# Kernel tuning notes

Measured on AMD Instinct MI355X. Metric: run time of the kernel, lower is better.

## Reference

```python
import jax, jax.numpy as jnp
import numpy as np

V, NJ, NSHAPE, NEXP, B = 5023, 5, 100, 50, 1024
PARENTS = np.array([-1, 0, 1, 1, 1])  # FLAME kinematic tree: global, neck, jaw, eyeL, eyeR


def rodrigues(rot_vecs):
    """Axis-angle [..., 3] -> rotation matrices [..., 3, 3] (SMPL-style, eps-safe)."""
    angle = jnp.linalg.norm(rot_vecs + 1e-8, axis=-1, keepdims=True)  # [...,1]
    axis = rot_vecs / angle
    cos = jnp.cos(angle)[..., None]
    sin = jnp.sin(angle)[..., None]
    rx, ry, rz = axis[..., 0], axis[..., 1], axis[..., 2]
    z = jnp.zeros_like(rx)
    K = jnp.stack([z, -rz, ry, rz, z, -rx, -ry, rx, z], axis=-1).reshape(rot_vecs.shape[:-1] + (3, 3))
    eye = jnp.eye(3, dtype=rot_vecs.dtype)
    return eye + sin * K + (1.0 - cos) * (K @ K)


def setup_inputs() -> dict:
    ks = jax.random.split(jax.random.key(0), 8)
    shape_params = jax.random.normal(ks[0], (B, NSHAPE), jnp.float32)
    expression_params = jax.random.normal(ks[1], (B, NEXP), jnp.float32)
    pose_params = 0.1 * jax.random.normal(ks[2], (B, 6), jnp.float32)
    v_template = jax.random.normal(ks[3], (V, 3), jnp.float32)
    shapedirs = 0.01 * jax.random.normal(ks[4], (V, 3, NSHAPE + NEXP), jnp.float32)
    posedirs = 0.01 * jax.random.normal(ks[5], ((NJ - 1) * 9, V * 3), jnp.float32)
    jr = jax.random.uniform(ks[6], (NJ, V), jnp.float32)
    J_regressor = jr / jr.sum(axis=1, keepdims=True)
    w = jax.random.uniform(ks[7], (V, NJ), jnp.float32)
    lbs_weights = w / w.sum(axis=1, keepdims=True)
    return dict(shape_params=shape_params, expression_params=expression_params,
                pose_params=pose_params, v_template=v_template, shapedirs=shapedirs,
                posedirs=posedirs, J_regressor=J_regressor, lbs_weights=lbs_weights)


def reference(shape_params, expression_params, pose_params, v_template,
              shapedirs, posedirs, J_regressor, lbs_weights):
    b = shape_params.shape[0]
    dt = shape_params.dtype
    # full_pose = [global(3), neck(3)=0, jaw(3), eyes(6)=0]
    zeros3 = jnp.zeros((b, 3), dt)
    zeros6 = jnp.zeros((b, 6), dt)
    full_pose = jnp.concatenate([pose_params[:, :3], zeros3, pose_params[:, 3:], zeros6], axis=1)
    betas = jnp.concatenate([shape_params, expression_params], axis=1)  # [b, 150]

    # shape blendshapes
    v_shaped = v_template[None] + jnp.einsum('bl,vcl->bvc', betas, shapedirs)  # [b,V,3]
    joints = jnp.einsum('jv,bvc->bjc', J_regressor, v_shaped)                 # [b,J,3]

    # pose blendshapes
    rot_mats = rodrigues(full_pose.reshape(b, NJ, 3))                         # [b,J,3,3]
    eye3 = jnp.eye(3, dtype=dt)
    pose_feature = (rot_mats[:, 1:] - eye3).reshape(b, (NJ - 1) * 9)
    v_posed = v_shaped + (pose_feature @ posedirs).reshape(b, V, 3)

    # rigid kinematic chain
    rel_joints = joints.at[:, 1:].add(-joints[:, PARENTS[1:]])                # [b,J,3]
    bottom = jnp.broadcast_to(jnp.array([0.0, 0.0, 0.0, 1.0], dt), (b, NJ, 1, 4))
    tmats = jnp.concatenate([jnp.concatenate([rot_mats, rel_joints[..., None]], axis=-1), bottom], axis=-2)  # [b,J,4,4]
    chain = [tmats[:, 0]]
    for i in range(1, NJ):  # fixed 5-joint tree
        chain.append(chain[PARENTS[i]] @ tmats[:, i])
    transforms = jnp.stack(chain, axis=1)                                     # [b,J,4,4]
    joints_h = jnp.concatenate([joints, jnp.zeros((b, NJ, 1), dt)], axis=-1)[..., None]  # [b,J,4,1]
    rel_transforms = transforms - jnp.pad(transforms @ joints_h, ((0, 0), (0, 0), (0, 0), (3, 0)))  # [b,J,4,4]

    # linear blend skinning
    T = jnp.einsum('vj,bjxy->bvxy', lbs_weights, rel_transforms)              # [b,V,4,4]
    v_h = jnp.concatenate([v_posed, jnp.ones((b, V, 1), dt)], axis=-1)        # [b,V,4]
    vertices = jnp.einsum('bvxy,bvy->bvx', T, v_h)[..., :3]                   # [b,V,3]
    return vertices, T
```

## Files before the change

kernel.cpp:

```cpp
#include <hip/hip_runtime.h>

#define VN     5023
#define NBETA  150
#define NBP    152
#define NBATCH 1024
#define N3     15069
#define BT     16
#define K1_CHUNK 40

__global__ void k0_pad(const float* __restrict__ sd, const float* __restrict__ vt,
                       float* __restrict__ sdp, float* __restrict__ JS) {
    int i = blockIdx.x * 256 + threadIdx.x;
    if (i < 15 * NBP) JS[i] = 0.0f;
    if (i >= N3 * NBP) return;
    int row = i / NBP, l = i - row * NBP;
    float val = 0.0f;
    if (l < NBETA) val = sd[row * NBETA + l];
    else if (l == NBETA) val = vt[row];
    sdp[i] = val;
}

__global__ void k1_js(const float* __restrict__ jr, const float* __restrict__ sdp,
                      float* __restrict__ JS) {
    int j3c = blockIdx.x;
    int j = j3c / 3, c = j3c - 3 * j;
    int l = threadIdx.x;
    if (l >= NBP) return;
    int v0 = blockIdx.y * K1_CHUNK, v1 = min(v0 + K1_CHUNK, VN);
    float acc = 0.0f;
    for (int v = v0; v < v1; ++v)
        acc += jr[j * VN + v] * sdp[(size_t)(v * 3 + c) * NBP + l];
    atomicAdd(&JS[j3c * NBP + l], acc);
}

__device__ __forceinline__ void rodrigues3(float x, float y, float z, float* R) {
    float ax = x + 1e-8f, ay = y + 1e-8f, az = z + 1e-8f;
    float ang = sqrtf(ax * ax + ay * ay + az * az);
    float inv = 1.0f / ang;
    float ux = x * inv, uy = y * inv, uz = z * inv;
    float co = cosf(ang), si = sinf(ang), t1 = 1.0f - co;
    float K[9] = {0.f, -uz, uy,  uz, 0.f, -ux,  -uy, ux, 0.f};
    float K2[9];
#pragma unroll
    for (int r = 0; r < 3; r++)
#pragma unroll
        for (int cc = 0; cc < 3; cc++) {
            float a = 0.f;
#pragma unroll
            for (int k = 0; k < 3; k++) a += K[r * 3 + k] * K[k * 3 + cc];
            K2[r * 3 + cc] = a;
        }
#pragma unroll
    for (int i = 0; i < 9; i++) {
        float e = (i == 0 || i == 4 || i == 8) ? 1.f : 0.f;
        R[i] = e + si * K[i] + t1 * K2[i];
    }
}

__global__ void k2_pose(const float* __restrict__ shp, const float* __restrict__ expr,
                        const float* __restrict__ pose, const float* __restrict__ JS,
                        float* __restrict__ betasF, float* __restrict__ pf9,
                        float* __restrict__ rel) {
    int b = blockIdx.x;
    int tt = threadIdx.x;
    __shared__ float sB[NBP];
    __shared__ float sJ[15];
    for (int l = tt; l < NBP; l += 64) {
        float val = 0.0f;
        if (l < 100) val = shp[b * 100 + l];
        else if (l < 150) val = expr[b * 50 + (l - 100)];
        else if (l == 150) val = 1.0f;
        sB[l] = val;
        betasF[b * NBP + l] = val;
    }
    __syncthreads();
    if (tt < 15) {
        float acc = 0.0f;
        const float* row = JS + tt * NBP;
        for (int l = 0; l < NBP; ++l) acc += row[l] * sB[l];
        sJ[tt] = acc;
    }
    __syncthreads();
    if (tt == 0) {
        float p[6];
#pragma unroll
        for (int i = 0; i < 6; i++) p[i] = pose[b * 6 + i];
        float R0[9], RJ[9];
        rodrigues3(p[0], p[1], p[2], R0);
        rodrigues3(p[3], p[4], p[5], RJ);
        float Jm[5][3];
#pragma unroll
        for (int jj = 0; jj < 5; jj++)
#pragma unroll
            for (int cc = 0; cc < 3; cc++) Jm[jj][cc] = sJ[jj * 3 + cc];
        float rj[5][3];
#pragma unroll
        for (int cc = 0; cc < 3; cc++) {
            rj[0][cc] = Jm[0][cc];
            rj[1][cc] = Jm[1][cc] - Jm[0][cc];
            rj[2][cc] = Jm[2][cc] - Jm[1][cc];
            rj[3][cc] = Jm[3][cc] - Jm[1][cc];
            rj[4][cc] = Jm[4][cc] - Jm[1][cc];
        }
        float tw[5][3];
#pragma unroll
        for (int cc = 0; cc < 3; cc++) tw[0][cc] = rj[0][cc];
#pragma unroll
        for (int cc = 0; cc < 3; cc++)
            tw[1][cc] = R0[cc * 3 + 0] * rj[1][0] + R0[cc * 3 + 1] * rj[1][1] + R0[cc * 3 + 2] * rj[1][2] + tw[0][cc];
#pragma unroll
        for (int jj = 2; jj < 5; jj++)
#pragma unroll
            for (int cc = 0; cc < 3; cc++)
                tw[jj][cc] = R0[cc * 3 + 0] * rj[jj][0] + R0[cc * 3 + 1] * rj[jj][1] + R0[cc * 3 + 2] * rj[jj][2] + tw[1][cc];
        float R2w[9];
#pragma unroll
        for (int r = 0; r < 3; r++)
#pragma unroll
            for (int cc = 0; cc < 3; cc++) {
                float a = 0.f;
#pragma unroll
                for (int k = 0; k < 3; k++) a += R0[r * 3 + k] * RJ[k * 3 + cc];
                R2w[r * 3 + cc] = a;
            }
        float* ro = rel + b * 80;
#pragma unroll
        for (int jj = 0; jj < 5; jj++) {
            const float* Rw = (jj == 2) ? R2w : R0;
#pragma unroll
            for (int rr = 0; rr < 3; rr++) {
                ro[jj * 16 + rr * 4 + 0] = Rw[rr * 3 + 0];
                ro[jj * 16 + rr * 4 + 1] = Rw[rr * 3 + 1];
                ro[jj * 16 + rr * 4 + 2] = Rw[rr * 3 + 2];
                float tj = Rw[rr * 3 + 0] * Jm[jj][0] + Rw[rr * 3 + 1] * Jm[jj][1] + Rw[rr * 3 + 2] * Jm[jj][2];
                ro[jj * 16 + rr * 4 + 3] = tw[jj][rr] - tj;
            }
            ro[jj * 16 + 12] = 0.f; ro[jj * 16 + 13] = 0.f; ro[jj * 16 + 14] = 0.f; ro[jj * 16 + 15] = 1.f;
        }
        float* pf = pf9 + b * 12;
#pragma unroll
        for (int e = 0; e < 9; e++) pf[e] = RJ[e] - ((e == 0 || e == 4 || e == 8) ? 1.f : 0.f);
        pf[9] = 0.f; pf[10] = 0.f; pf[11] = 0.f;
    }
}

__global__ void __launch_bounds__(128, 2)
k3_main(const float* __restrict__ sdp, const float* __restrict__ pd,
        const float* __restrict__ lw,
        const float* __restrict__ betasF, const float* __restrict__ pf9,
        const float* __restrict__ rel,
        float* __restrict__ outv, float* __restrict__ outT) {
    __shared__ float sBet[BT][NBP];
    __shared__ float sRel[BT][80];
    __shared__ float sPf[BT][12];

    int tid = threadIdx.x;
    int v = blockIdx.x * 128 + tid;
    bool ok = v < VN;
    int vc = ok ? v : VN - 1;
    int b0 = blockIdx.y * BT;

    for (int i = tid; i < BT * NBP; i += 128) {
        int bb = i / NBP, l = i - bb * NBP;
        sBet[bb][l] = betasF[(size_t)(b0 + bb) * NBP + l];
    }
    for (int i = tid; i < BT * 80; i += 128) {
        int bb = i / 80, e = i - bb * 80;
        sRel[bb][e] = rel[(size_t)(b0 + bb) * 80 + e];
    }
    for (int i = tid; i < BT * 12; i += 128) {
        int bb = i / 12, e = i - bb * 12;
        sPf[bb][e] = pf9[(size_t)(b0 + bb) * 12 + e];
    }
    __syncthreads();

    float acc[3][BT];
#pragma unroll
    for (int c = 0; c < 3; c++)
#pragma unroll
        for (int bb = 0; bb < BT; bb++) acc[c][bb] = 0.0f;

    const float* srow = sdp + (size_t)vc * 3 * NBP;

#pragma unroll 1
    for (int l0 = 0; l0 < NBP; l0 += 8) {
        const float4 a0  = *(const float4*)(srow + l0);
        const float4 a1  = *(const float4*)(srow + l0 + 4);
        const float4 bq0 = *(const float4*)(srow + NBP + l0);
        const float4 bq1 = *(const float4*)(srow + NBP + l0 + 4);
        const float4 cq0 = *(const float4*)(srow + 2 * NBP + l0);
        const float4 cq1 = *(const float4*)(srow + 2 * NBP + l0 + 4);
        float s0[8] = {a0.x, a0.y, a0.z, a0.w, a1.x, a1.y, a1.z, a1.w};
        float s1[8] = {bq0.x, bq0.y, bq0.z, bq0.w, bq1.x, bq1.y, bq1.z, bq1.w};
        float s2[8] = {cq0.x, cq0.y, cq0.z, cq0.w, cq1.x, cq1.y, cq1.z, cq1.w};
#pragma unroll
        for (int bb = 0; bb < BT; bb++) {
            const float4 be0 = *(const float4*)(&sBet[bb][l0]);
            const float4 be1 = *(const float4*)(&sBet[bb][l0 + 4]);
            float be[8] = {be0.x, be0.y, be0.z, be0.w, be1.x, be1.y, be1.z, be1.w};
#pragma unroll
            for (int k = 0; k < 8; k++) {
                acc[0][bb] += be[k] * s0[k];
                acc[1][bb] += be[k] * s1[k];
                acc[2][bb] += be[k] * s2[k];
            }
        }
    }

    if (!ok) return;

    float wj[5], pdv[9][3];
#pragma unroll
    for (int j = 0; j < 5; j++) wj[j] = lw[v * 5 + j];
#pragma unroll
    for (int k = 0; k < 9; k++)
#pragma unroll
        for (int c = 0; c < 3; c++) pdv[k][c] = pd[(size_t)(9 + k) * N3 + v * 3 + c];

#pragma unroll
    for (int bb = 0; bb < BT; bb++) {
        int b = b0 + bb;
        float vp[3];
#pragma unroll
        for (int c = 0; c < 3; c++) {
            float x = acc[c][bb];
#pragma unroll
            for (int k = 0; k < 9; k++) x += sPf[bb][k] * pdv[k][c];
            vp[c] = x;
        }
        float T[16];
#pragma unroll
        for (int e = 0; e < 16; e++) T[e] = 0.0f;
#pragma unroll
        for (int j = 0; j < 5; j++) {
            float w = wj[j];
            const float4* rj4 = (const float4*)(&sRel[bb][j * 16]);
            float4 r0 = rj4[0], r1 = rj4[1], r2 = rj4[2], r3 = rj4[3];
            T[0]  += w * r0.x;  T[1]  += w * r0.y;  T[2]  += w * r0.z;  T[3]  += w * r0.w;
            T[4]  += w * r1.x;  T[5]  += w * r1.y;  T[6]  += w * r1.z;  T[7]  += w * r1.w;
            T[8]  += w * r2.x;  T[9]  += w * r2.y;  T[10] += w * r2.z;  T[11] += w * r2.w;
            T[12] += w * r3.x;  T[13] += w * r3.y;  T[14] += w * r3.z;  T[15] += w * r3.w;
        }
        float vo[3];
#pragma unroll
        for (int rr = 0; rr < 3; rr++)
            vo[rr] = T[rr * 4 + 0] * vp[0] + T[rr * 4 + 1] * vp[1] + T[rr * 4 + 2] * vp[2] + T[rr * 4 + 3];

        size_t vbase = (size_t)b * VN + v;
        float* pv = outv + vbase * 3;
        pv[0] = vo[0];
        pv[1] = vo[1];
        pv[2] = vo[2];
        float4* pT = (float4*)(outT + vbase * 16);
        pT[0] = make_float4(T[0],  T[1],  T[2],  T[3]);
        pT[1] = make_float4(T[4],  T[5],  T[6],  T[7]);
        pT[2] = make_float4(T[8],  T[9],  T[10], T[11]);
        pT[3] = make_float4(T[12], T[13], T[14], T[15]);
    }
}

extern "C" void kernel_launch(void* const* d_in, const int* in_sizes, int n_in,
                              void* d_out, int out_size, void* d_ws, size_t ws_size,
                              hipStream_t stream) {
    const float* shp  = (const float*)d_in[0];
    const float* expr = (const float*)d_in[1];
    const float* pose = (const float*)d_in[2];
    const float* vt   = (const float*)d_in[3];
    const float* sd   = (const float*)d_in[4];
    const float* pd   = (const float*)d_in[5];
    const float* jr   = (const float*)d_in[6];
    const float* lw   = (const float*)d_in[7];

    float* outv = (float*)d_out;
    float* outT = outv + (size_t)NBATCH * VN * 3;

    char* w = (char*)d_ws;
    const size_t SDP_B   = (size_t)N3 * NBP * 4;
    const size_t JS_B    = 15 * NBP * 4;
    const size_t BETAS_B = (size_t)NBATCH * NBP * 4;
    const size_t PF9_B   = (size_t)NBATCH * 12 * 4;
    float* sdp    = (float*)w;
    float* JS     = (float*)(w + SDP_B);
    float* betasF = (float*)(w + SDP_B + JS_B);
    float* pf9    = (float*)(w + SDP_B + JS_B + BETAS_B);
    float* rel    = (float*)(w + SDP_B + JS_B + BETAS_B + PF9_B);

    k0_pad<<<(N3 * NBP + 255) / 256, 256, 0, stream>>>(sd, vt, sdp, JS);
    k1_js<<<dim3(15, (VN + K1_CHUNK - 1) / K1_CHUNK), 192, 0, stream>>>(jr, sdp, JS);
    k2_pose<<<NBATCH, 64, 0, stream>>>(shp, expr, pose, JS, betasF, pf9, rel);
    k3_main<<<dim3(40, NBATCH / BT), 128, 0, stream>>>(sdp, pd, lw, betasF, pf9, rel, outv, outT);
}
```

Before: 245.1 us.

## Transpose padded shapedirs to float4-by-vertex layout for coalesced main-kernel loads

Result: faster. 239.0 us (-2.5%).

```diff
diff --git a/kernel.cpp b/kernel.cpp
--- a/kernel.cpp
+++ b/kernel.cpp
@@ -3,34 +3,62 @@
 #define VN     5023
 #define NBETA  150
 #define NBP    152
+#define NL4    38
+#define VP     5024
 #define NBATCH 1024
 #define N3     15069
 #define BT     16
-#define K1_CHUNK 40
-
-__global__ void k0_pad(const float* __restrict__ sd, const float* __restrict__ vt,
-                       float* __restrict__ sdp, float* __restrict__ JS) {
+
+__global__ void k0_t4(const float* __restrict__ sd, const float* __restrict__ vt,
+                      float4* __restrict__ sdpT4) {
     int i = blockIdx.x * 256 + threadIdx.x;
-    if (i < 15 * NBP) JS[i] = 0.0f;
-    if (i >= N3 * NBP) return;
-    int row = i / NBP, l = i - row * NBP;
-    float val = 0.0f;
-    if (l < NBETA) val = sd[row * NBETA + l];
-    else if (l == NBETA) val = vt[row];
-    sdp[i] = val;
-}
-
-__global__ void k1_js(const float* __restrict__ jr, const float* __restrict__ sdp,
+    if (i >= 3 * NL4 * VP) return;
+    int c   = i / (NL4 * VP);
+    int rem = i - c * (NL4 * VP);
+    int l4  = rem / VP;
+    int v   = rem - l4 * VP;
+    float4 out = make_float4(0.f, 0.f, 0.f, 0.f);
+    if (v < VN) {
+        int row = v * 3 + c;
+        float vals[4];
+#pragma unroll
+        for (int q = 0; q < 4; q++) {
+            int ll = l4 * 4 + q;
+            vals[q] = (ll < NBETA) ? sd[row * NBETA + ll]
+                     : ((ll == NBETA) ? vt[row] : 0.f);
+        }
+        out = make_float4(vals[0], vals[1], vals[2], vals[3]);
+    }
+    sdpT4[i] = out;
+}
+
+__global__ void k1_t4(const float* __restrict__ jr, const float4* __restrict__ sdpT4,
                       float* __restrict__ JS) {
-    int j3c = blockIdx.x;
+    int j3c = blockIdx.x, l4 = blockIdx.y;
     int j = j3c / 3, c = j3c - 3 * j;
-    int l = threadIdx.x;
-    if (l >= NBP) return;
-    int v0 = blockIdx.y * K1_CHUNK, v1 = min(v0 + K1_CHUNK, VN);
-    float acc = 0.0f;
-    for (int v = v0; v < v1; ++v)
-        acc += jr[j * VN + v] * sdp[(size_t)(v * 3 + c) * NBP + l];
-    atomicAdd(&JS[j3c * NBP + l], acc);
+    int t = threadIdx.x;
+    const float4* col = sdpT4 + (size_t)(c * NL4 + l4) * VP;
+    float4 acc = make_float4(0.f, 0.f, 0.f, 0.f);
+    for (int v = t; v < VN; v += 256) {
+        float w = jr[j * VN + v];
+        float4 s = col[v];
+        acc.x += w * s.x; acc.y += w * s.y; acc.z += w * s.z; acc.w += w * s.w;
+    }
+    __shared__ float4 red[256];
+    red[t] = acc; __syncthreads();
+    for (int s = 128; s > 0; s >>= 1) {
+        if (t < s) {
+            red[t].x += red[t + s].x; red[t].y += red[t + s].y;
+            red[t].z += red[t + s].z; red[t].w += red[t + s].w;
+        }
+        __syncthreads();
+    }
+    if (t == 0) {
+        JS[j3c * NBP + l4 * 4 + 0] = red[0].x;
+        JS[j3c * NBP + l4 * 4 + 1] = red[0].y;
+        JS[j3c * NBP + l4 * 4 + 2] = red[0].z;
+        JS[j3c * NBP + l4 * 4 + 3] = red[0].w;
+    }
 }
 
 __device__ __forceinline__ void rodrigues3(float x, float y, float z, float* R) {
@@ -145,7 +173,7 @@
 }
 
 __global__ void __launch_bounds__(128, 2)
-k3_main(const float* __restrict__ sdp, const float* __restrict__ pd,
+k3_main(const float4* __restrict__ sdpT4, const float* __restrict__ pd,
         const float* __restrict__ lw,
         const float* __restrict__ betasF, const float* __restrict__ pf9,
         const float* __restrict__ rel,
@@ -180,19 +208,20 @@
 #pragma unroll
         for (int bb = 0; bb < BT; bb++) acc[c][bb] = 0.0f;
 
-    const float* srow = sdp + (size_t)vc * 3 * NBP;
+    const float4* sp = sdpT4 + vc;
 
 #pragma unroll 1
     for (int l0 = 0; l0 < NBP; l0 += 8) {
-        const float4 a0  = *(const float4*)(srow + l0);
-        const float4 a1  = *(const float4*)(srow + l0 + 4);
-        const float4 bq0 = *(const float4*)(srow + NBP + l0);
-        const float4 bq1 = *(const float4*)(srow + NBP + l0 + 4);
-        const float4 cq0 = *(const float4*)(srow + 2 * NBP + l0);
-        const float4 cq1 = *(const float4*)(srow + 2 * NBP + l0 + 4);
+        int i0 = l0 >> 2;
+        const float4 a0 = sp[(size_t)(0 * NL4 + i0) * VP];
+        const float4 a1 = sp[(size_t)(0 * NL4 + i0 + 1) * VP];
+        const float4 b0q = sp[(size_t)(1 * NL4 + i0) * VP];
+        const float4 b1q = sp[(size_t)(1 * NL4 + i0 + 1) * VP];
+        const float4 c0q = sp[(size_t)(2 * NL4 + i0) * VP];
+        const float4 c1q = sp[(size_t)(2 * NL4 + i0 + 1) * VP];
         float s0[8] = {a0.x, a0.y, a0.z, a0.w, a1.x, a1.y, a1.z, a1.w};
-        float s1[8] = {bq0.x, bq0.y, bq0.z, bq0.w, bq1.x, bq1.y, bq1.z, bq1.w};
-        float s2[8] = {cq0.x, cq0.y, cq0.z, cq0.w, cq1.x, cq1.y, cq1.z, cq1.w};
+        float s1[8] = {b0q.x, b0q.y, b0q.z, b0q.w, b1q.x, b1q.y, b1q.z, b1q.w};
+        float s2[8] = {c0q.x, c0q.y, c0q.z, c0q.w, c1q.x, c1q.y, c1q.z, c1q.w};
 #pragma unroll
         for (int bb = 0; bb < BT; bb++) {
             const float4 be0 = *(const float4*)(&sBet[bb][l0]);
@@ -275,18 +304,18 @@
     float* outT = outv + (size_t)NBATCH * VN * 3;
 
     char* w = (char*)d_ws;
-    const size_t SDP_B   = (size_t)N3 * NBP * 4;
+    const size_t SDPT_B  = (size_t)3 * NL4 * VP * 16;
     const size_t JS_B    = 15 * NBP * 4;
     const size_t BETAS_B = (size_t)NBATCH * NBP * 4;
     const size_t PF9_B   = (size_t)NBATCH * 12 * 4;
-    float* sdp    = (float*)w;
-    float* JS     = (float*)(w + SDP_B);
-    float* betasF = (float*)(w + SDP_B + JS_B);
-    float* pf9    = (float*)(w + SDP_B + JS_B + BETAS_B);
-    float* rel    = (float*)(w + SDP_B + JS_B + BETAS_B + PF9_B);
-
-    k0_pad<<<(N3 * NBP + 255) / 256, 256, 0, stream>>>(sd, vt, sdp, JS);
-    k1_js<<<dim3(15, (VN + K1_CHUNK - 1) / K1_CHUNK), 192, 0, stream>>>(jr, sdp, JS);
+    float4* sdpT4 = (float4*)w;
+    float* JS     = (float*)(w + SDPT_B);
+    float* betasF = (float*)(w + SDPT_B + JS_B);
+    float* pf9    = (float*)(w + SDPT_B + JS_B + BETAS_B);
+    float* rel    = (float*)(w + SDPT_B + JS_B + BETAS_B + PF9_B);
+
+    k0_t4<<<(3 * NL4 * VP + 255) / 256, 256, 0, stream>>>(sd, vt, sdpT4);
+    k1_t4<<<dim3(15, NL4), 256, 0, stream>>>(jr, sdpT4, JS);
     k2_pose<<<NBATCH, 64, 0, stream>>>(shp, expr, pose, JS, betasF, pf9, rel);
-    k3_main<<<dim3(40, NBATCH / BT), 128, 0, stream>>>(sdp, pd, lw, betasF, pf9, rel, outv, outT);
-}
+    k3_main<<<dim3(40, NBATCH / BT), 128, 0, stream>>>(sdpT4, pd, lw, betasF, pf9, rel, outv, outT);
+}
```
